# Optimization experiments

Measured on AMD Instinct MI355X. Metric: run time of the kernel, lower is better.

## Reference

```python
import jax, jax.numpy as jnp
import numpy as np

# G graphs of K atoms each, fully connected within graph (no self loops)
G, K, L, H, F, EMB, HID = 256, 16, 3, 3, 64, 200, 256
N = G * K
E = G * K * (K - 1)


def _wap(x, index, weights, num_seg, pw, gW1, gb1, gW2, gb2, mW1, mb1, mW2, mb2):
    """Roost WeightedAttentionPooling: segment softmax of gate_nn(x), scaled by
    weights**pow, applied to message_nn(x), segment-summed."""
    gate = jax.nn.selu(x @ gW1 + gb1) @ gW2 + gb2                      # [M]
    gmax = jax.ops.segment_max(gate, index, num_segments=num_seg)      # [S]
    gate = jnp.power(weights, pw) * jnp.exp(gate - gmax[index])        # [M]
    den = jax.ops.segment_sum(gate, index, num_segments=num_seg) + 1e-10
    attn = gate / den[index]                                           # [M]
    msg = jax.nn.selu(x @ mW1 + mb1) @ mW2 + mb2                       # [M,F]
    return jax.ops.segment_sum(attn[:, None] * msg, index, num_segments=num_seg)


def _wap_heads(x, index, weights, num_seg, params):
    f = lambda pw, gW1, gb1, gW2, gb2, mW1, mb1, mW2, mb2: _wap(
        x, index, weights, num_seg, pw, gW1, gb1, gW2, gb2, mW1, mb1, mW2, mb2)
    return jax.vmap(f)(*params)                                        # [H,S,F]


def setup_inputs() -> dict:
    key = jax.random.key(0)
    ks = jax.random.split(key, 16)
    # graph structure
    batch = jnp.repeat(jnp.arange(G, dtype=jnp.int32), K)              # [N]
    i = np.arange(K)
    src, dst = np.meshgrid(i, i, indexing="ij")
    mask = src != dst
    src, dst = src[mask], dst[mask]                                    # [K*(K-1)]
    offs = (np.arange(G) * K)[:, None]
    self_idx = jnp.asarray((offs + src[None, :]).reshape(-1), jnp.int32)
    nbr_idx = jnp.asarray((offs + dst[None, :]).reshape(-1), jnp.int32)

    s = lambda k, shape, fan_in: jax.random.normal(k, shape, jnp.float32) * (1.0 / fan_in) ** 0.5
    return dict(
        elem_weights=jax.random.uniform(ks[0], (N,), jnp.float32, 0.01, 1.0),
        elem_fea_in=jax.random.normal(ks[1], (N, EMB), jnp.float32),
        W_init=s(ks[2], (EMB, F - 1), EMB),
        b_init=jnp.zeros((F - 1,), jnp.float32),
        mg_W1=s(ks[3], (L, H, 2 * F, HID), 2 * F),
        mg_b1=jnp.zeros((L, H, HID), jnp.float32),
        mg_W2=s(ks[4], (L, H, HID), HID),
        mg_b2=jnp.zeros((L, H), jnp.float32),
        mm_W1=s(ks[5], (L, H, 2 * F, HID), 2 * F),
        mm_b1=jnp.zeros((L, H, HID), jnp.float32),
        mm_W2=s(ks[6], (L, H, HID, F), HID),
        mm_b2=jnp.zeros((L, H, F), jnp.float32),
        m_pow=jax.random.normal(ks[7], (L, H), jnp.float32),
        cg_W1=s(ks[8], (H, F, HID), F),
        cg_b1=jnp.zeros((H, HID), jnp.float32),
        cg_W2=s(ks[9], (H, HID), HID),
        cg_b2=jnp.zeros((H,), jnp.float32),
        cm_W1=s(ks[10], (H, F, HID), F),
        cm_b1=jnp.zeros((H, HID), jnp.float32),
        cm_W2=s(ks[11], (H, HID, F), HID),
        cm_b2=jnp.zeros((H, F), jnp.float32),
        c_pow=jax.random.normal(ks[12], (H,), jnp.float32),
        batch=batch,
        self_idx=self_idx,
        nbr_idx=nbr_idx,
    )


def reference(elem_weights, elem_fea_in, W_init, b_init,
              mg_W1, mg_b1, mg_W2, mg_b2, mm_W1, mm_b1, mm_W2, mm_b2, m_pow,
              cg_W1, cg_b1, cg_W2, cg_b2, cm_W1, cm_b1, cm_W2, cm_b2, c_pow,
              batch, self_idx, nbr_idx):
    w = elem_weights                                                   # [N]
    # initial embed: Linear(EMB, F-1) then concat fractional weight
    fea = jnp.concatenate([elem_fea_in @ W_init + b_init, w[:, None]], -1)  # [N,F]
    wn = w[nbr_idx]                                                    # [E]
    for l in range(L):
        pair = jnp.concatenate([fea[self_idx], fea[nbr_idx]], -1)      # [E,2F]
        heads = _wap_heads(pair, self_idx, wn, N,
                           (m_pow[l], mg_W1[l], mg_b1[l], mg_W2[l], mg_b2[l],
                            mm_W1[l], mm_b1[l], mm_W2[l], mm_b2[l]))   # [H,N,F]
        fea = fea + heads.mean(0)                                      # residual
    cry = _wap_heads(fea, batch, w, G,
                     (c_pow, cg_W1, cg_b1, cg_W2, cg_b2,
                      cm_W1, cm_b1, cm_W2, cm_b2))                     # [H,G,F]
    return cry.mean(0)                                                 # [G,F]
```

## Files before the change

kernel.cpp:

```cpp
#include <hip/hip_runtime.h>
#include <hip/hip_bf16.h>

#define G_ 256
#define K_ 16
#define L_ 3
#define H_ 3
#define F_ 64
#define EMB_ 200
#define HID_ 256
#define N_ (G_*K_)

typedef __attribute__((ext_vector_type(8))) short short8;
typedef __attribute__((ext_vector_type(4))) float f32x4;

#define SELU_S 1.0507009873554804934193349852946f
#define SELU_SA (1.0507009873554804934193349852946f*1.6732632423543772848170429916717f)
#define LOG2E_ 1.4426950408889634073599246810019f
#define SLN2_ (SELU_S*0.69314718055994530941723212145818f)

__device__ __forceinline__ float exp2_fast(float x) {
#if __has_builtin(__builtin_amdgcn_exp2f)
  return __builtin_amdgcn_exp2f(x);
#else
  return __exp2f(x);
#endif
}

__device__ __forceinline__ float selu_t(float t) {
  float tn = fminf(t, 0.f), tp = fmaxf(t, 0.f);
  return fmaf(SELU_SA, exp2_fast(tn), fmaf(SLN2_, tp, -SELU_SA));
}

__device__ __forceinline__ float selu_f(float x) {
  float e = __expf(x);
  float neg = fmaf(SELU_SA, e, -SELU_SA);
  float pos = SELU_S * x;
  return x > 0.f ? pos : neg;
}

__device__ __forceinline__ unsigned short f2bf(float x) {
  __hip_bfloat16 h = __float2bfloat16(x);
  return *reinterpret_cast<unsigned short*>(&h);
}

__device__ __forceinline__ unsigned int f2bf2(float a, float b) {
  float2 t; t.x = a; t.y = b;
  __hip_bfloat162 h = __float22bfloat162_rn(t);
  return *reinterpret_cast<unsigned int*>(&h);
}

__device__ __forceinline__ float bf2f(unsigned short u) {
  union { unsigned int i; float f; } v;
  v.i = ((unsigned int)u) << 16;
  return v.f;
}

__global__ __launch_bounds__(256) void prep_init_all(
    const float* __restrict__ mg_W1, const float* __restrict__ mm_W1,
    const float* __restrict__ mm_W2, const float* __restrict__ cg_W1,
    const float* __restrict__ cm_W1, const float* __restrict__ cm_W2,
    const float* __restrict__ mg_b1, const float* __restrict__ mm_b1,
    const float* __restrict__ cg_b1, const float* __restrict__ cm_b1,
    unsigned short* __restrict__ WcatT, unsigned short* __restrict__ W2mT,
    unsigned short* __restrict__ WcryT, unsigned short* __restrict__ W2cT,
    float* __restrict__ bias_e, float* __restrict__ bias_c,
    float* __restrict__ out0, float* __restrict__ feaZ,
    const float* __restrict__ fea_in, const float* __restrict__ W_init,
    const float* __restrict__ b_init, const float* __restrict__ wts,
    float* __restrict__ feaA) {
  int bid = blockIdx.x, tid = threadIdx.x;
  if (bid >= 256) {
    __shared__ float row[4][EMB_];
    int sub = tid >> 6, j = tid & 63;
    int n = (bid - 256) * 4 + sub;
    for (int k = j; k < EMB_; k += 64) row[sub][k] = fea_in[(size_t)n*EMB_ + k];
    __syncthreads();
    if (j < F_-1) {
      float s = b_init[j];
      for (int k = 0; k < EMB_; ++k) s = fmaf(row[sub][k], W_init[k*(F_-1) + j], s);
      feaA[(size_t)n*F_ + j] = s;
    } else {
      feaA[(size_t)n*F_ + (F_-1)] = wts[n];
    }
    return;
  }
  int gt = bid*256 + tid, GT = 256*256;
  for (int idx = gt; idx < 9*1024*64; idx += GT) {
    int lh = idx >> 16, n = (idx >> 6) & 1023, k = idx & 63;
    const float* W = (n < 512) ? mg_W1 : mm_W1;
    int nn = n & 511;
    int r = (nn < 256) ? k : (64 + k);
    WcatT[idx] = f2bf(W[(size_t)lh*(2*F_*HID_) + r*HID_ + (nn & 255)]);
  }
  for (int idx = gt; idx < 9*64*256; idx += GT) {
    int lh = idx >> 14, f = (idx >> 8) & 63, k = idx & 255;
    W2mT[idx] = f2bf(mm_W2[(size_t)lh*(HID_*F_) + k*F_ + f]);
  }
  for (int idx = gt; idx < 1536*64; idx += GT) {
    int n = idx >> 6, k = idx & 63;
    int hh = n >> 9, r = n & 511;
    float v = (r < 256) ? cg_W1[(size_t)hh*F_*HID_ + k*HID_ + r]
                        : cm_W1[(size_t)hh*F_*HID_ + k*HID_ + (r - 256)];
    WcryT[idx] = f2bf(v);
  }
  for (int idx = gt; idx < 3*64*256; idx += GT) {
    int hh = idx >> 14, f = (idx >> 8) & 63, k = idx & 255;
    W2cT[idx] = f2bf(cm_W2[(size_t)hh*HID_*F_ + k*F_ + f]);
  }
  for (int idx = gt; idx < 9216 + 1536 + G_*F_; idx += GT) {
    if (idx < 9216) {
      int l = idx / 3072, c = idx - l*3072;
      int hh = c >> 10, cc = c & 1023;
      int lh = l*H_ + hh;
      float v = 0.f;
      if (cc < 256) v = mg_b1[lh*HID_ + cc];
      else if (cc >= 512 && cc < 768) v = mm_b1[lh*HID_ + (cc - 512)];
      bias_e[idx] = v;
    } else if (idx < 9216 + 1536) {
      int c = idx - 9216;
      int hh = c >> 9, cc = c & 511;
      bias_c[c] = (cc < 256) ? cg_b1[hh*HID_ + cc] : cm_b1[hh*HID_ + (cc - 256)];
    } else {
      out0[idx - 9216 - 1536] = 0.f;
    }
  }
  float4 z4; z4.x = 0.f; z4.y = 0.f; z4.z = 0.f; z4.w = 0.f;
  for (int idx = gt; idx < (3*N_*F_)/4; idx += GT)
    ((float4*)feaZ)[idx] = z4;
}

__global__ __launch_bounds__(512, 4) void edge_fused(
    const float* __restrict__ fea, const unsigned short* __restrict__ WcatT,
    const float* __restrict__ bias_e, const unsigned short* __restrict__ W2T,
    const float* __restrict__ mg_W2, const float* __restrict__ mg_b2,
    const float* __restrict__ m_pow, const float* __restrict__ mm_b2,
    const float* __restrict__ wts, float* __restrict__ fea_nxt, int l) {
  __shared__ __align__(16) unsigned short feaS[16][72];
  __shared__ __align__(16) unsigned short PQs[16][520];
  __shared__ __align__(16) unsigned short HbarS[16][264];
  __shared__ float bs[512];
  __shared__ float w2g[256];
  __shared__ float gred[240][2];
  __shared__ float gateA[240];
  __shared__ float sumat[16];
  __shared__ float wp[16];
  int t = threadIdx.x;
  int g = blockIdx.x, g16 = g * 16;
  int h = blockIdx.y, lh = l*H_ + h;
  const unsigned short* Wlh = WcatT + (size_t)lh*1024*64;
  const float* biaslh = bias_e + (size_t)l*3072 + h*1024;
  int w = t >> 6, lane = t & 63, mr = lane & 15, q = lane >> 4;

  {
    int row = t >> 5, c2 = (t & 31) * 2;
    float2 fv = *(const float2*)&fea[(size_t)(g16 + row)*64 + c2];
    *(unsigned int*)&feaS[row][c2] = f2bf2(fv.x, fv.y);
  }
  bs[t] = biaslh[t];
  if (t < 256) w2g[t] = mg_W2[lh*HID_ + t];
  __syncthreads();

  {
    int n0w = w * 64;
    short8 a0 = *(const short8*)&feaS[mr][q*8];
    short8 a1 = *(const short8*)&feaS[mr][32 + q*8];
    #pragma unroll
    for (int nt = 0; nt < 4; ++nt) {
      int n = n0w + nt*16 + mr;
      const unsigned short* bp = Wlh + (size_t)n*64 + q*8;
      short8 b0 = *(const short8*)bp;
      short8 b1 = *(const short8*)(bp + 32);
      f32x4 z = {0.f, 0.f, 0.f, 0.f};
      z = __builtin_amdgcn_mfma_f32_16x16x32_bf16(a0, b0, z, 0, 0, 0);
      z = __builtin_amdgcn_mfma_f32_16x16x32_bf16(a1, b1, z, 0, 0, 0);
      float bb = bs[n];
      #pragma unroll
      for (int r = 0; r < 4; ++r)
        PQs[q*4 + r][n] = f2bf(z[r] + bb);
    }
  }
  __syncthreads();

  {
    float nb = biaslh[512 + t];
    if (t < 480) {
      int e = t >> 1, half = t & 1;
      int i = e / 15, jj = e - i*15;
      int j = (jj < i) ? jj : jj + 1;
      float s = 0.f;
      #pragma unroll
      for (int u = 0; u < 16; ++u) {
        int c = half*8 + u*16;
        short8 pv = *(const short8*)&PQs[i][c];
        short8 qv = *(const short8*)&PQs[j][256 + c];
        #pragma unroll
        for (int r = 0; r < 8; ++r) {
          float hv = selu_f(bf2f((unsigned short)pv[r]) + bf2f((unsigned short)qv[r]));
          s = fmaf(hv, w2g[c + r], s);
        }
      }
      gred[e][half] = s;
    } else if (t < 496) {
      wp[t - 480] = __powf(wts[g16 + (t - 480)], m_pow[lh]);
    }
    bs[t] = nb;
  }
  __syncthreads();

  {
    int n0w = w * 64;
    short8 a0 = *(const short8*)&feaS[mr][q*8];
    short8 a1 = *(const short8*)&feaS[mr][32 + q*8];
    #pragma unroll
    for (int nt = 0; nt < 4; ++nt) {
      int n = n0w + nt*16 + mr;
      const unsigned short* bp = Wlh + (size_t)(512 + n)*64 + q*8;
      short8 b0 = *(const short8*)bp;
      short8 b1 = *(const short8*)(bp + 32);
      f32x4 z = {0.f, 0.f, 0.f, 0.f};
      z = __builtin_amdgcn_mfma_f32_16x16x32_bf16(a0, b0, z, 0, 0, 0);
      z = __builtin_amdgcn_mfma_f32_16x16x32_bf16(a1, b1, z, 0, 0, 0);
      float bb = bs[n];
      #pragma unroll
      for (int r = 0; r < 4; ++r)
        PQs[q*4 + r][n] = f2bf(z[r] + bb);
    }
  }
  if (t < 16) {
    int i = t;
    float b2v = mg_b2[lh];
    float gl[15];
    float m = -1e30f;
    #pragma unroll
    for (int jj = 0; jj < 15; ++jj) {
      float v = gred[i*15 + jj][0] + gred[i*15 + jj][1] + b2v;
      gl[jj] = v; m = fmaxf(m, v);
    }
    float den = 0.f;
    #pragma unroll
    for (int jj = 0; jj < 15; ++jj) {
      int j = (jj < i) ? jj : jj + 1;
      float x = wp[j] * __expf(gl[jj] - m);
      gl[jj] = x; den += x;
    }
    den += 1e-10f;
    float sa = 0.f;
    #pragma unroll
    for (int jj = 0; jj < 15; ++jj) {
      float a = gl[jj] / den; gateA[i*15 + jj] = a; sa += a;
    }
    sumat[i] = sa;
  }
  __syncthreads();

  {
    int i = t >> 5, k0 = (t & 31) * 8;
    short8 pv = *(const short8*)&PQs[i][k0];
    float pf[8];
    #pragma unroll
    for (int r = 0; r < 8; ++r) pf[r] = bf2f((unsigned short)pv[r]);
    float hb[8] = {0.f, 0.f, 0.f, 0.f, 0.f, 0.f, 0.f, 0.f};
    for (int jj = 0; jj < 15; ++jj) {
      int j = (jj < i) ? jj : jj + 1;
      float a = gateA[i*15 + jj];
      short8 qv = *(const short8*)&PQs[j][256 + k0];
      #pragma unroll
      for (int r = 0; r < 8; ++r) {
        float hv = selu_f(pf[r] + bf2f((unsigned short)qv[r]));
        hb[r] = fmaf(a, hv, hb[r]);
      }
    }
    unsigned int hpk[4];
    #pragma unroll
    for (int r2 = 0; r2 < 4; ++r2) hpk[r2] = f2bf2(hb[2*r2], hb[2*r2+1]);
    *(short8*)&HbarS[i][k0] = *reinterpret_cast<short8*>(hpk);
  }
  __syncthreads();

  if (w < 4) {
    const unsigned short* W2lh = W2T + (size_t)lh*64*256;
    f32x4 acc = {0.f, 0.f, 0.f, 0.f};
    #pragma unroll
    for (int kc = 0; kc < 8; ++kc) {
      short8 a = *(const short8*)&HbarS[mr][kc*32 + q*8];
      short8 b = *(const short8*)&W2lh[(size_t)(w*16 + mr)*256 + kc*32 + q*8];
      acc = __builtin_amdgcn_mfma_f32_16x16x32_bf16(a, b, acc, 0, 0, 0);
    }
    int f = w*16 + mr;
    float b2 = mm_b2[lh*F_ + f];
    #pragma unroll
    for (int r = 0; r < 4; ++r) {
      int i = q*4 + r;
      float val = (acc[r] + b2*sumat[i]) * (1.f/3.f);
      if (h == 0) val += fea[(size_t)(g16 + i)*64 + f];
      atomicAdd(&fea_nxt[(size_t)(g16 + i)*64 + f], val);
    }
  }
}

__global__ __launch_bounds__(256) void cry_fused(
    const float* __restrict__ fea, const unsigned short* __restrict__ WcryT,
    const float* __restrict__ bias_c, const unsigned short* __restrict__ W2cT,
    const float* __restrict__ cg_W2, const float* __restrict__ cg_b2,
    const float* __restrict__ cm_b2, const float* __restrict__ c_pow,
    const float* __restrict__ wts, float* __restrict__ out) {
  __shared__ __align__(16) unsigned short feaS[16][72];
  __shared__ float PQh[16][520];
  __shared__ float bsc[512];
  __shared__ float gred[16][18];
  __shared__ float attnL[16];
  __shared__ float sumatS;
  __shared__ __align__(16) unsigned short hidc[16][264];
  int t = threadIdx.x;
  int g = blockIdx.x, g16 = g*16, h = blockIdx.y;
  {
    int row = t >> 4, c4 = (t & 15) * 4;
    float4 fv = *(const float4*)&fea[(size_t)(g16 + row)*64 + c4];
    *(unsigned int*)&feaS[row][c4]   = f2bf2(fv.x, fv.y);
    *(unsigned int*)&feaS[row][c4+2] = f2bf2(fv.z, fv.w);
  }
  bsc[t] = bias_c[h*512 + t];
  bsc[256 + t] = bias_c[h*512 + 256 + t];
  int w = t >> 6, lane = t & 63, mr = lane & 15, q = lane >> 4;
  __syncthreads();
  {
    int n0w = w * 128;
    short8 a0 = *(const short8*)&feaS[mr][q*8];
    short8 a1 = *(const short8*)&feaS[mr][32 + q*8];
    #pragma unroll
    for (int nt = 0; nt < 8; ++nt) {
      int n = n0w + nt*16 + mr;
      const unsigned short* bp = WcryT + (size_t)(h*512 + n)*64 + q*8;
      short8 b0 = *(const short8*)bp;
      short8 b1 = *(const short8*)(bp + 32);
      f32x4 z = {0.f, 0.f, 0.f, 0.f};
      z = __builtin_amdgcn_mfma_f32_16x16x32_bf16(a0, b0, z, 0, 0, 0);
      z = __builtin_amdgcn_mfma_f32_16x16x32_bf16(a1, b1, z, 0, 0, 0);
      float bb = bsc[n];
      #pragma unroll
      for (int r = 0; r < 4; ++r)
        PQh[q*4 + r][n] = (z[r] + bb) * LOG2E_;
    }
  }
  __syncthreads();
  {
    int i = t >> 4, c0 = (t & 15) * 16;
    float s = 0.f;
    #pragma unroll
    for (int c = c0; c < c0+16; ++c)
      s = fmaf(selu_t(PQh[i][c]), cg_W2[h*HID_ + c], s);
    gred[i][t & 15] = s;
  }
  __syncthreads();
  if (t < 16) {
    float sg = 0.f;
    #pragma unroll
    for (int u2 = 0; u2 < 16; ++u2) sg += gred[t][u2];
    gred[t][16] = sg + cg_b2[h];
  }
  __syncthreads();
  if (t == 0) {
    float pw = c_pow[h];
    float m = -1e30f;
    #pragma unroll
    for (int i = 0; i < 16; ++i) m = fmaxf(m, gred[i][16]);
    float den = 0.f; float v[16];
    #pragma unroll
    for (int i = 0; i < 16; ++i) {
      float x = __powf(wts[g16+i], pw) * __expf(gred[i][16] - m);
      v[i] = x; den += x;
    }
    den += 1e-10f;
    float sa = 0.f;
    #pragma unroll
    for (int i = 0; i < 16; ++i) { float a = v[i]/den; attnL[i] = a; sa += a; }
    sumatS = sa;
  }
  {
    int i = t >> 4, c0 = (t & 15) * 16;
    #pragma unroll
    for (int c = c0; c < c0+16; c += 2) {
      unsigned int pk = f2bf2(selu_t(PQh[i][256 + c]), selu_t(PQh[i][256 + c + 1]));
      *(unsigned int*)&hidc[i][c] = pk;
    }
  }
  __syncthreads();
  f32x4 acc = {0.f, 0.f, 0.f, 0.f};
  #pragma unroll
  for (int kc = 0; kc < 8; ++kc) {
    short8 a = *(const short8*)&hidc[mr][kc*32 + q*8];
    short8 b = *(const short8*)&W2cT[((size_t)h*64 + w*16 + mr)*HID_ + kc*32 + q*8];
    acc = __builtin_amdgcn_mfma_f32_16x16x32_bf16(a, b, acc, 0, 0, 0);
  }
  float p = 0.f;
  #pragma unroll
  for (int r = 0; r < 4; ++r) p = fmaf(attnL[q*4+r], acc[r], p);
  p += __shfl_xor(p, 16);
  p += __shfl_xor(p, 32);
  if (q == 0) {
    int f = w*16 + mr;
    atomicAdd(&out[(size_t)g*64 + f],
              (p + cm_b2[h*F_ + f]*sumatS) * (1.f/(float)H_));
  }
}

extern "C" void kernel_launch(void* const* d_in, const int* in_sizes, int n_in,
                              void* d_out, int out_size, void* d_ws, size_t ws_size,
                              hipStream_t stream) {
  const float* elem_weights = (const float*)d_in[0];
  const float* elem_fea_in  = (const float*)d_in[1];
  const float* W_init = (const float*)d_in[2];
  const float* b_init = (const float*)d_in[3];
  const float* mg_W1  = (const float*)d_in[4];
  const float* mg_b1  = (const float*)d_in[5];
  const float* mg_W2  = (const float*)d_in[6];
  const float* mg_b2  = (const float*)d_in[7];
  const float* mm_W1  = (const float*)d_in[8];
  const float* mm_b1  = (const float*)d_in[9];
  const float* mm_W2  = (const float*)d_in[10];
  const float* mm_b2  = (const float*)d_in[11];
  const float* m_pow  = (const float*)d_in[12];
  const float* cg_W1  = (const float*)d_in[13];
  const float* cg_b1  = (const float*)d_in[14];
  const float* cg_W2  = (const float*)d_in[15];
  const float* cg_b2  = (const float*)d_in[16];
  const float* cm_W1  = (const float*)d_in[17];
  const float* cm_b1  = (const float*)d_in[18];
  const float* cm_W2  = (const float*)d_in[19];
  const float* cm_b2  = (const float*)d_in[20];
  const float* c_pow  = (const float*)d_in[21];
  float* out = (float*)d_out;

  float* ws = (float*)d_ws;
  float* feaA  = ws;
  float* feaB  = feaA + (size_t)N_*F_;
  float* feaC  = feaB + (size_t)N_*F_;
  float* feaD  = feaC + (size_t)N_*F_;
  unsigned short* WcatT = (unsigned short*)(feaD + (size_t)N_*F_);
  unsigned short* W2mT  = WcatT + (size_t)9*1024*64;
  unsigned short* WcryT = W2mT  + (size_t)9*64*256;
  unsigned short* W2cT  = WcryT + (size_t)1536*64;
  float* bias_e = (float*)(W2cT + (size_t)3*64*256);
  float* bias_c = bias_e + 9216;

  prep_init_all<<<256 + N_/4, 256, 0, stream>>>(
      mg_W1, mm_W1, mm_W2, cg_W1, cm_W1, cm_W2,
      mg_b1, mm_b1, cg_b1, cm_b1,
      WcatT, W2mT, WcryT, W2cT, bias_e, bias_c,
      out, feaB,
      elem_fea_in, W_init, b_init, elem_weights, feaA);

  float* bufs[4] = {feaA, feaB, feaC, feaD};
  for (int l = 0; l < L_; ++l) {
    edge_fused<<<dim3(G_, H_), 512, 0, stream>>>(
        bufs[l], WcatT, bias_e, W2mT, mg_W2, mg_b2, m_pow, mm_b2,
        elem_weights, bufs[l+1], l);
  }

  cry_fused<<<dim3(G_, H_), 256, 0, stream>>>(
      bufs[3], WcryT, bias_c, W2cT, cg_W2, cg_b2, cm_b2, c_pow,
      elem_weights, out);
}
```

Measured before the change: 235.7 us.

## Fuse edge layers and crystal pooling into one kernel with per-graph barriers

The three edge_fused launches and the cry_fused launch are merged into a single net_fused kernel. The three head blocks of each graph synchronise through a global atomic counter with spin-waiting, which removes kernel-launch gaps and tail effects between layers. The crystal stage is reworked to run with 512 threads, store its hidden activations in bf16 and compute the softmax with shuffles instead of a single thread. The prep kernel now spreads its weight-transpose loops across all blocks and zeroes the counters. The spin barrier relies on all blocks of a graph being resident at the same time, so it risks deadlock if occupancy is insufficient.

```diff
diff --git a/kernel.cpp b/kernel.cpp
--- a/kernel.cpp
+++ b/kernel.cpp
@@ -53,6 +53,18 @@
   union { unsigned int i; float f; } v;
   v.i = ((unsigned int)u) << 16;
   return v.f;
+}
+
+__device__ __forceinline__ void graph_barrier(unsigned int* c, int t) {
+  __syncthreads();
+  if (t == 0) {
+    __threadfence();
+    atomicAdd(c, 1u);
+    while (__hip_atomic_load(c, __ATOMIC_ACQUIRE, __HIP_MEMORY_SCOPE_AGENT) < 3u)
+      __builtin_amdgcn_s_sleep(8);
+  }
+  __syncthreads();
+  __threadfence();
 }
 
 __global__ __launch_bounds__(256) void prep_init_all(
@@ -67,7 +79,7 @@
     float* __restrict__ out0, float* __restrict__ feaZ,
     const float* __restrict__ fea_in, const float* __restrict__ W_init,
     const float* __restrict__ b_init, const float* __restrict__ wts,
-    float* __restrict__ feaA) {
+    float* __restrict__ feaA, unsigned int* __restrict__ cnt0) {
   int bid = blockIdx.x, tid = threadIdx.x;
   if (bid >= 256) {
     __shared__ float row[4][EMB_];
@@ -82,9 +94,8 @@
     } else {
       feaA[(size_t)n*F_ + (F_-1)] = wts[n];
     }
-    return;
-  }
-  int gt = bid*256 + tid, GT = 256*256;
+  }
+  int gt = bid*256 + tid, GT = gridDim.x*256;
   for (int idx = gt; idx < 9*1024*64; idx += GT) {
     int lh = idx >> 16, n = (idx >> 6) & 1023, k = idx & 63;
     const float* W = (n < 512) ? mg_W1 : mm_W1;
@@ -107,7 +118,7 @@
     int hh = idx >> 14, f = (idx >> 8) & 63, k = idx & 255;
     W2cT[idx] = f2bf(cm_W2[(size_t)hh*HID_*F_ + k*F_ + f]);
   }
-  for (int idx = gt; idx < 9216 + 1536 + G_*F_; idx += GT) {
+  for (int idx = gt; idx < 9216 + 1536 + G_*F_ + 1024; idx += GT) {
     if (idx < 9216) {
       int l = idx / 3072, c = idx - l*3072;
       int hh = c >> 10, cc = c & 1023;
@@ -120,8 +131,10 @@
       int c = idx - 9216;
       int hh = c >> 9, cc = c & 511;
       bias_c[c] = (cc < 256) ? cg_b1[hh*HID_ + cc] : cm_b1[hh*HID_ + (cc - 256)];
+    } else if (idx < 9216 + 1536 + G_*F_) {
+      out0[idx - 9216 - 1536] = 0.f;
     } else {
-      out0[idx - 9216 - 1536] = 0.f;
+      cnt0[idx - 9216 - 1536 - G_*F_] = 0u;
     }
   }
   float4 z4; z4.x = 0.f; z4.y = 0.f; z4.z = 0.f; z4.w = 0.f;
@@ -129,41 +142,54 @@
     ((float4*)feaZ)[idx] = z4;
 }
 
-__global__ __launch_bounds__(512, 4) void edge_fused(
-    const float* __restrict__ fea, const unsigned short* __restrict__ WcatT,
-    const float* __restrict__ bias_e, const unsigned short* __restrict__ W2T,
-    const float* __restrict__ mg_W2, const float* __restrict__ mg_b2,
-    const float* __restrict__ m_pow, const float* __restrict__ mm_b2,
-    const float* __restrict__ wts, float* __restrict__ fea_nxt, int l) {
-  __shared__ __align__(16) unsigned short feaS[16][72];
-  __shared__ __align__(16) unsigned short PQs[16][520];
-  __shared__ __align__(16) unsigned short HbarS[16][264];
-  __shared__ float bs[512];
-  __shared__ float w2g[256];
-  __shared__ float gred[240][2];
-  __shared__ float gateA[240];
-  __shared__ float sumat[16];
-  __shared__ float wp[16];
-  int t = threadIdx.x;
-  int g = blockIdx.x, g16 = g * 16;
-  int h = blockIdx.y, lh = l*H_ + h;
+struct EdgeSmem {
+  unsigned short feaS[16][72];
+  unsigned short PQs[16][520];
+  unsigned short HbarS[16][264];
+  float bs[512];
+  float w2g[256];
+  float gred[240][2];
+  float gateA[240];
+  float sumat[16];
+  float wp[16];
+};
+struct CrySmem {
+  unsigned short feaS[16][72];
+  unsigned short PQh[16][520];
+  unsigned short hidc[16][264];
+  float bsc[512];
+  float gred[16][36];
+  float attnL[16];
+  float sumatS;
+};
+union NetSmem { EdgeSmem e; CrySmem c; };
+
+__device__ __forceinline__ void do_layer(
+    NetSmem& S, int t, int g16, int h, int l,
+    const float* __restrict__ cur, float* __restrict__ nxt,
+    const unsigned short* __restrict__ WcatT, const float* __restrict__ bias_e,
+    const unsigned short* __restrict__ W2T, const float* __restrict__ mg_W2,
+    const float* __restrict__ mg_b2, const float* __restrict__ m_pow,
+    const float* __restrict__ mm_b2, const float* __restrict__ wts) {
+  EdgeSmem& e = S.e;
+  int lh = l*H_ + h;
   const unsigned short* Wlh = WcatT + (size_t)lh*1024*64;
   const float* biaslh = bias_e + (size_t)l*3072 + h*1024;
   int w = t >> 6, lane = t & 63, mr = lane & 15, q = lane >> 4;
 
   {
     int row = t >> 5, c2 = (t & 31) * 2;
-    float2 fv = *(const float2*)&fea[(size_t)(g16 + row)*64 + c2];
-    *(unsigned int*)&feaS[row][c2] = f2bf2(fv.x, fv.y);
-  }
-  bs[t] = biaslh[t];
-  if (t < 256) w2g[t] = mg_W2[lh*HID_ + t];
+    float2 fv = *(const float2*)&cur[(size_t)(g16 + row)*64 + c2];
+    *(unsigned int*)&e.feaS[row][c2] = f2bf2(fv.x, fv.y);
+  }
+  e.bs[t] = biaslh[t];
+  if (t < 256) e.w2g[t] = mg_W2[lh*HID_ + t];
   __syncthreads();
 
   {
     int n0w = w * 64;
-    short8 a0 = *(const short8*)&feaS[mr][q*8];
-    short8 a1 = *(const short8*)&feaS[mr][32 + q*8];
+    short8 a0 = *(const short8*)&e.feaS[mr][q*8];
+    short8 a1 = *(const short8*)&e.feaS[mr][32 + q*8];
     #pragma unroll
     for (int nt = 0; nt < 4; ++nt) {
       int n = n0w + nt*16 + mr;
@@ -173,10 +199,10 @@
       f32x4 z = {0.f, 0.f, 0.f, 0.f};
       z = __builtin_amdgcn_mfma_f32_16x16x32_bf16(a0, b0, z, 0, 0, 0);
       z = __builtin_amdgcn_mfma_f32_16x16x32_bf16(a1, b1, z, 0, 0, 0);
-      float bb = bs[n];
+      float bb = e.bs[n];
       #pragma unroll
       for (int r = 0; r < 4; ++r)
-        PQs[q*4 + r][n] = f2bf(z[r] + bb);
+        e.PQs[q*4 + r][n] = f2bf(z[r] + bb);
     }
   }
   __syncthreads();
@@ -184,33 +210,33 @@
   {
     float nb = biaslh[512 + t];
     if (t < 480) {
-      int e = t >> 1, half = t & 1;
-      int i = e / 15, jj = e - i*15;
+      int ed = t >> 1, half = t & 1;
+      int i = ed / 15, jj = ed - i*15;
       int j = (jj < i) ? jj : jj + 1;
       float s = 0.f;
       #pragma unroll
       for (int u = 0; u < 16; ++u) {
         int c = half*8 + u*16;
-        short8 pv = *(const short8*)&PQs[i][c];
-        short8 qv = *(const short8*)&PQs[j][256 + c];
+        short8 pv = *(const short8*)&e.PQs[i][c];
+        short8 qv = *(const short8*)&e.PQs[j][256 + c];
         #pragma unroll
         for (int r = 0; r < 8; ++r) {
           float hv = selu_f(bf2f((unsigned short)pv[r]) + bf2f((unsigned short)qv[r]));
-          s = fmaf(hv, w2g[c + r], s);
+          s = fmaf(hv, e.w2g[c + r], s);
         }
       }
-      gred[e][half] = s;
+      e.gred[ed][half] = s;
     } else if (t < 496) {
-      wp[t - 480] = __powf(wts[g16 + (t - 480)], m_pow[lh]);
-    }
-    bs[t] = nb;
+      e.wp[t - 480] = __powf(wts[g16 + (t - 480)], m_pow[lh]);
+    }
+    e.bs[t] = nb;
   }
   __syncthreads();
 
   {
     int n0w = w * 64;
-    short8 a0 = *(const short8*)&feaS[mr][q*8];
-    short8 a1 = *(const short8*)&feaS[mr][32 + q*8];
+    short8 a0 = *(const short8*)&e.feaS[mr][q*8];
+    short8 a1 = *(const short8*)&e.feaS[mr][32 + q*8];
     #pragma unroll
     for (int nt = 0; nt < 4; ++nt) {
       int n = n0w + nt*16 + mr;
@@ -220,10 +246,10 @@
       f32x4 z = {0.f, 0.f, 0.f, 0.f};
       z = __builtin_amdgcn_mfma_f32_16x16x32_bf16(a0, b0, z, 0, 0, 0);
       z = __builtin_amdgcn_mfma_f32_16x16x32_bf16(a1, b1, z, 0, 0, 0);
-      float bb = bs[n];
+      float bb = e.bs[n];
       #pragma unroll
       for (int r = 0; r < 4; ++r)
-        PQs[q*4 + r][n] = f2bf(z[r] + bb);
+        e.PQs[q*4 + r][n] = f2bf(z[r] + bb);
     }
   }
   if (t < 16) {
@@ -233,37 +259,37 @@
     float m = -1e30f;
     #pragma unroll
     for (int jj = 0; jj < 15; ++jj) {
-      float v = gred[i*15 + jj][0] + gred[i*15 + jj][1] + b2v;
+      float v = e.gred[i*15 + jj][0] + e.gred[i*15 + jj][1] + b2v;
       gl[jj] = v; m = fmaxf(m, v);
     }
     float den = 0.f;
     #pragma unroll
     for (int jj = 0; jj < 15; ++jj) {
       int j = (jj < i) ? jj : jj + 1;
-      float x = wp[j] * __expf(gl[jj] - m);
+      float x = e.wp[j] * __expf(gl[jj] - m);
       gl[jj] = x; den += x;
     }
     den += 1e-10f;
     float sa = 0.f;
     #pragma unroll
     for (int jj = 0; jj < 15; ++jj) {
-      float a = gl[jj] / den; gateA[i*15 + jj] = a; sa += a;
-    }
-    sumat[i] = sa;
+      float a = gl[jj] / den; e.gateA[i*15 + jj] = a; sa += a;
+    }
+    e.sumat[i] = sa;
   }
   __syncthreads();
 
   {
     int i = t >> 5, k0 = (t & 31) * 8;
-    short8 pv = *(const short8*)&PQs[i][k0];
+    short8 pv = *(const short8*)&e.PQs[i][k0];
     float pf[8];
     #pragma unroll
     for (int r = 0; r < 8; ++r) pf[r] = bf2f((unsigned short)pv[r]);
     float hb[8] = {0.f, 0.f, 0.f, 0.f, 0.f, 0.f, 0.f, 0.f};
     for (int jj = 0; jj < 15; ++jj) {
       int j = (jj < i) ? jj : jj + 1;
-      float a = gateA[i*15 + jj];
-      short8 qv = *(const short8*)&PQs[j][256 + k0];
+      float a = e.gateA[i*15 + jj];
+      short8 qv = *(const short8*)&e.PQs[j][256 + k0];
       #pragma unroll
       for (int r = 0; r < 8; ++r) {
         float hv = selu_f(pf[r] + bf2f((unsigned short)qv[r]));
@@ -273,7 +299,7 @@
     unsigned int hpk[4];
     #pragma unroll
     for (int r2 = 0; r2 < 4; ++r2) hpk[r2] = f2bf2(hb[2*r2], hb[2*r2+1]);
-    *(short8*)&HbarS[i][k0] = *reinterpret_cast<short8*>(hpk);
+    *(short8*)&e.HbarS[i][k0] = *reinterpret_cast<short8*>(hpk);
   }
   __syncthreads();
 
@@ -282,7 +308,7 @@
     f32x4 acc = {0.f, 0.f, 0.f, 0.f};
     #pragma unroll
     for (int kc = 0; kc < 8; ++kc) {
-      short8 a = *(const short8*)&HbarS[mr][kc*32 + q*8];
+      short8 a = *(const short8*)&e.HbarS[mr][kc*32 + q*8];
       short8 b = *(const short8*)&W2lh[(size_t)(w*16 + mr)*256 + kc*32 + q*8];
       acc = __builtin_amdgcn_mfma_f32_16x16x32_bf16(a, b, acc, 0, 0, 0);
     }
@@ -291,44 +317,36 @@
     #pragma unroll
     for (int r = 0; r < 4; ++r) {
       int i = q*4 + r;
-      float val = (acc[r] + b2*sumat[i]) * (1.f/3.f);
-      if (h == 0) val += fea[(size_t)(g16 + i)*64 + f];
-      atomicAdd(&fea_nxt[(size_t)(g16 + i)*64 + f], val);
-    }
-  }
-}
-
-__global__ __launch_bounds__(256) void cry_fused(
+      float val = (acc[r] + b2*e.sumat[i]) * (1.f/3.f);
+      if (h == 0) val += cur[(size_t)(g16 + i)*64 + f];
+      atomicAdd(&nxt[(size_t)(g16 + i)*64 + f], val);
+    }
+  }
+}
+
+__device__ __forceinline__ void do_cry(
+    NetSmem& S, int t, int g, int h,
     const float* __restrict__ fea, const unsigned short* __restrict__ WcryT,
     const float* __restrict__ bias_c, const unsigned short* __restrict__ W2cT,
     const float* __restrict__ cg_W2, const float* __restrict__ cg_b2,
     const float* __restrict__ cm_b2, const float* __restrict__ c_pow,
     const float* __restrict__ wts, float* __restrict__ out) {
-  __shared__ __align__(16) unsigned short feaS[16][72];
-  __shared__ float PQh[16][520];
-  __shared__ float bsc[512];
-  __shared__ float gred[16][18];
-  __shared__ float attnL[16];
-  __shared__ float sumatS;
-  __shared__ __align__(16) unsigned short hidc[16][264];
-  int t = threadIdx.x;
-  int g = blockIdx.x, g16 = g*16, h = blockIdx.y;
-  {
-    int row = t >> 4, c4 = (t & 15) * 4;
-    float4 fv = *(const float4*)&fea[(size_t)(g16 + row)*64 + c4];
-    *(unsigned int*)&feaS[row][c4]   = f2bf2(fv.x, fv.y);
-    *(unsigned int*)&feaS[row][c4+2] = f2bf2(fv.z, fv.w);
-  }
-  bsc[t] = bias_c[h*512 + t];
-  bsc[256 + t] = bias_c[h*512 + 256 + t];
+  CrySmem& c = S.c;
+  int g16 = g*16;
   int w = t >> 6, lane = t & 63, mr = lane & 15, q = lane >> 4;
-  __syncthreads();
-  {
-    int n0w = w * 128;
-    short8 a0 = *(const short8*)&feaS[mr][q*8];
-    short8 a1 = *(const short8*)&feaS[mr][32 + q*8];
-    #pragma unroll
-    for (int nt = 0; nt < 8; ++nt) {
+  {
+    int row = t >> 5, c2 = (t & 31) * 2;
+    float2 fv = *(const float2*)&fea[(size_t)(g16 + row)*64 + c2];
+    *(unsigned int*)&c.feaS[row][c2] = f2bf2(fv.x, fv.y);
+  }
+  c.bsc[t] = bias_c[h*512 + t];
+  __syncthreads();
+  {
+    int n0w = w * 64;
+    short8 a0 = *(const short8*)&c.feaS[mr][q*8];
+    short8 a1 = *(const short8*)&c.feaS[mr][32 + q*8];
+    #pragma unroll
+    for (int nt = 0; nt < 4; ++nt) {
       int n = n0w + nt*16 + mr;
       const unsigned short* bp = WcryT + (size_t)(h*512 + n)*64 + q*8;
       short8 b0 = *(const short8*)bp;
@@ -336,72 +354,98 @@
       f32x4 z = {0.f, 0.f, 0.f, 0.f};
       z = __builtin_amdgcn_mfma_f32_16x16x32_bf16(a0, b0, z, 0, 0, 0);
       z = __builtin_amdgcn_mfma_f32_16x16x32_bf16(a1, b1, z, 0, 0, 0);
-      float bb = bsc[n];
+      float bb = c.bsc[n];
       #pragma unroll
       for (int r = 0; r < 4; ++r)
-        PQh[q*4 + r][n] = (z[r] + bb) * LOG2E_;
-    }
-  }
-  __syncthreads();
-  {
-    int i = t >> 4, c0 = (t & 15) * 16;
+        c.PQh[q*4 + r][n] = f2bf((z[r] + bb) * LOG2E_);
+    }
+  }
+  __syncthreads();
+  {
+    int i = t >> 5, c0 = (t & 31) * 8;
     float s = 0.f;
     #pragma unroll
-    for (int c = c0; c < c0+16; ++c)
-      s = fmaf(selu_t(PQh[i][c]), cg_W2[h*HID_ + c], s);
-    gred[i][t & 15] = s;
+    for (int cc = c0; cc < c0+8; ++cc)
+      s = fmaf(selu_t(bf2f(c.PQh[i][cc])), cg_W2[h*HID_ + cc], s);
+    c.gred[i][t & 31] = s;
   }
   __syncthreads();
   if (t < 16) {
     float sg = 0.f;
     #pragma unroll
-    for (int u2 = 0; u2 < 16; ++u2) sg += gred[t][u2];
-    gred[t][16] = sg + cg_b2[h];
-  }
-  __syncthreads();
-  if (t == 0) {
-    float pw = c_pow[h];
-    float m = -1e30f;
-    #pragma unroll
-    for (int i = 0; i < 16; ++i) m = fmaxf(m, gred[i][16]);
-    float den = 0.f; float v[16];
-    #pragma unroll
-    for (int i = 0; i < 16; ++i) {
-      float x = __powf(wts[g16+i], pw) * __expf(gred[i][16] - m);
-      v[i] = x; den += x;
-    }
-    den += 1e-10f;
-    float sa = 0.f;
-    #pragma unroll
-    for (int i = 0; i < 16; ++i) { float a = v[i]/den; attnL[i] = a; sa += a; }
-    sumatS = sa;
-  }
-  {
-    int i = t >> 4, c0 = (t & 15) * 16;
-    #pragma unroll
-    for (int c = c0; c < c0+16; c += 2) {
-      unsigned int pk = f2bf2(selu_t(PQh[i][256 + c]), selu_t(PQh[i][256 + c + 1]));
-      *(unsigned int*)&hidc[i][c] = pk;
-    }
-  }
-  __syncthreads();
-  f32x4 acc = {0.f, 0.f, 0.f, 0.f};
-  #pragma unroll
-  for (int kc = 0; kc < 8; ++kc) {
-    short8 a = *(const short8*)&hidc[mr][kc*32 + q*8];
-    short8 b = *(const short8*)&W2cT[((size_t)h*64 + w*16 + mr)*HID_ + kc*32 + q*8];
-    acc = __builtin_amdgcn_mfma_f32_16x16x32_bf16(a, b, acc, 0, 0, 0);
-  }
-  float p = 0.f;
-  #pragma unroll
-  for (int r = 0; r < 4; ++r) p = fmaf(attnL[q*4+r], acc[r], p);
-  p += __shfl_xor(p, 16);
-  p += __shfl_xor(p, 32);
-  if (q == 0) {
-    int f = w*16 + mr;
-    atomicAdd(&out[(size_t)g*64 + f],
-              (p + cm_b2[h*F_ + f]*sumatS) * (1.f/(float)H_));
-  }
+    for (int u = 0; u < 32; ++u) sg += c.gred[t][u];
+    sg += cg_b2[h];
+    float m = sg;
+    #pragma unroll
+    for (int s = 1; s < 16; s <<= 1) m = fmaxf(m, __shfl_xor(m, s, 16));
+    float x = __powf(wts[g16 + t], c_pow[h]) * __expf(sg - m);
+    float d = x;
+    #pragma unroll
+    for (int s = 1; s < 16; s <<= 1) d += __shfl_xor(d, s, 16);
+    d += 1e-10f;
+    float a = x / d;
+    c.attnL[t] = a;
+    float sa = a;
+    #pragma unroll
+    for (int s = 1; s < 16; s <<= 1) sa += __shfl_xor(sa, s, 16);
+    if (t == 0) c.sumatS = sa;
+  }
+  {
+    int i = t >> 5, c0 = (t & 31) * 8;
+    #pragma unroll
+    for (int cc = c0; cc < c0+8; cc += 2) {
+      unsigned int pk = f2bf2(selu_t(bf2f(c.PQh[i][256 + cc])),
+                              selu_t(bf2f(c.PQh[i][256 + cc + 1])));
+      *(unsigned int*)&c.hidc[i][cc] = pk;
+    }
+  }
+  __syncthreads();
+  if (w < 4) {
+    f32x4 acc = {0.f, 0.f, 0.f, 0.f};
+    #pragma unroll
+    for (int kc = 0; kc < 8; ++kc) {
+      short8 a = *(const short8*)&c.hidc[mr][kc*32 + q*8];
+      short8 b = *(const short8*)&W2cT[((size_t)h*64 + w*16 + mr)*HID_ + kc*32 + q*8];
+      acc = __builtin_amdgcn_mfma_f32_16x16x32_bf16(a, b, acc, 0, 0, 0);
+    }
+    float p = 0.f;
+    #pragma unroll
+    for (int r = 0; r < 4; ++r) p = fmaf(c.attnL[q*4+r], acc[r], p);
+    p += __shfl_xor(p, 16);
+    p += __shfl_xor(p, 32);
+    if (q == 0) {
+      int f = w*16 + mr;
+      atomicAdd(&out[(size_t)g*64 + f],
+                (p + cm_b2[h*F_ + f]*c.sumatS) * (1.f/(float)H_));
+    }
+  }
+}
+
+__global__ __launch_bounds__(512, 8) void net_fused(
+    const float* __restrict__ fea0, float* __restrict__ fea1,
+    float* __restrict__ fea2, float* __restrict__ fea3,
+    const unsigned short* __restrict__ WcatT, const float* __restrict__ bias_e,
+    const unsigned short* __restrict__ W2mT, const float* __restrict__ mg_W2,
+    const float* __restrict__ mg_b2, const float* __restrict__ m_pow,
+    const float* __restrict__ mm_b2,
+    const unsigned short* __restrict__ WcryT, const float* __restrict__ bias_c,
+    const unsigned short* __restrict__ W2cT, const float* __restrict__ cg_W2,
+    const float* __restrict__ cg_b2, const float* __restrict__ cm_b2,
+    const float* __restrict__ c_pow,
+    const float* __restrict__ wts, float* __restrict__ out,
+    unsigned int* __restrict__ cnt) {
+  __shared__ __align__(16) NetSmem sm;
+  int t = threadIdx.x;
+  int g = blockIdx.x, g16 = g*16;
+  int h = blockIdx.y;
+
+  do_layer(sm, t, g16, h, 0, fea0, fea1, WcatT, bias_e, W2mT, mg_W2, mg_b2, m_pow, mm_b2, wts);
+  graph_barrier(&cnt[g*4 + 0], t);
+  do_layer(sm, t, g16, h, 1, fea1, fea2, WcatT, bias_e, W2mT, mg_W2, mg_b2, m_pow, mm_b2, wts);
+  graph_barrier(&cnt[g*4 + 1], t);
+  do_layer(sm, t, g16, h, 2, fea2, fea3, WcatT, bias_e, W2mT, mg_W2, mg_b2, m_pow, mm_b2, wts);
+  graph_barrier(&cnt[g*4 + 2], t);
+  do_cry(sm, t, g, h, fea3, WcryT, bias_c, W2cT, cg_W2, cg_b2, cm_b2, c_pow, wts, out);
 }
 
 extern "C" void kernel_launch(void* const* d_in, const int* in_sizes, int n_in,
@@ -442,22 +486,18 @@
   unsigned short* W2cT  = WcryT + (size_t)1536*64;
   float* bias_e = (float*)(W2cT + (size_t)3*64*256);
   float* bias_c = bias_e + 9216;
+  unsigned int* cnt = (unsigned int*)(bias_c + 1536);
 
   prep_init_all<<<256 + N_/4, 256, 0, stream>>>(
       mg_W1, mm_W1, mm_W2, cg_W1, cm_W1, cm_W2,
       mg_b1, mm_b1, cg_b1, cm_b1,
       WcatT, W2mT, WcryT, W2cT, bias_e, bias_c,
       out, feaB,
-      elem_fea_in, W_init, b_init, elem_weights, feaA);
-
-  float* bufs[4] = {feaA, feaB, feaC, feaD};
-  for (int l = 0; l < L_; ++l) {
-    edge_fused<<<dim3(G_, H_), 512, 0, stream>>>(
-        bufs[l], WcatT, bias_e, W2mT, mg_W2, mg_b2, m_pow, mm_b2,
-        elem_weights, bufs[l+1], l);
-  }
-
-  cry_fused<<<dim3(G_, H_), 256, 0, stream>>>(
-      bufs[3], WcryT, bias_c, W2cT, cg_W2, cg_b2, cm_b2, c_pow,
-      elem_weights, out);
-}
+      elem_fea_in, W_init, b_init, elem_weights, feaA, cnt);
+
+  net_fused<<<dim3(G_, H_), 512, 0, stream>>>(
+      feaA, feaB, feaC, feaD,
+      WcatT, bias_e, W2mT, mg_W2, mg_b2, m_pow, mm_b2,
+      WcryT, bias_c, W2cT, cg_W2, cg_b2, cm_b2, c_pow,
+      elem_weights, out, cnt);
+}
```

Result: slower. 694.8 us (+194.8%).

## Split edge kernel across two blocks per graph by target-atom halves

Applied to the files above, without the earlier changes.

Each graph/head is now handled by two 256-thread blocks, each owning 8 of the 16 target atoms, instead of one 512-thread block. Both blocks still compute the full P/Q projections, which are needed for every neighbor, so that GEMM work is duplicated. The pairwise gate, aggregation and output GEMM are halved per block, and the bias shared buffer is dropped in favor of direct global loads. The aim is more, smaller blocks for better occupancy and load balance. The cost is redundant projection compute and a half-empty 16-row MFMA in the final stage.

```diff
diff --git a/kernel.cpp b/kernel.cpp
--- a/kernel.cpp
+++ b/kernel.cpp
@@ -129,7 +129,7 @@
     ((float4*)feaZ)[idx] = z4;
 }
 
-__global__ __launch_bounds__(512, 4) void edge_fused(
+__global__ __launch_bounds__(256, 4) void edge_fused(
     const float* __restrict__ fea, const unsigned short* __restrict__ WcatT,
     const float* __restrict__ bias_e, const unsigned short* __restrict__ W2T,
     const float* __restrict__ mg_W2, const float* __restrict__ mg_b2,
@@ -137,35 +137,35 @@
     const float* __restrict__ wts, float* __restrict__ fea_nxt, int l) {
   __shared__ __align__(16) unsigned short feaS[16][72];
   __shared__ __align__(16) unsigned short PQs[16][520];
-  __shared__ __align__(16) unsigned short HbarS[16][264];
-  __shared__ float bs[512];
+  __shared__ __align__(16) unsigned short HbarS[8][264];
   __shared__ float w2g[256];
-  __shared__ float gred[240][2];
-  __shared__ float gateA[240];
-  __shared__ float sumat[16];
+  __shared__ float gred[120][2];
+  __shared__ float gateA[120];
+  __shared__ float sumat[8];
   __shared__ float wp[16];
   int t = threadIdx.x;
   int g = blockIdx.x, g16 = g * 16;
   int h = blockIdx.y, lh = l*H_ + h;
+  int i0 = blockIdx.z * 8;
   const unsigned short* Wlh = WcatT + (size_t)lh*1024*64;
   const float* biaslh = bias_e + (size_t)l*3072 + h*1024;
   int w = t >> 6, lane = t & 63, mr = lane & 15, q = lane >> 4;
 
   {
-    int row = t >> 5, c2 = (t & 31) * 2;
-    float2 fv = *(const float2*)&fea[(size_t)(g16 + row)*64 + c2];
-    *(unsigned int*)&feaS[row][c2] = f2bf2(fv.x, fv.y);
-  }
-  bs[t] = biaslh[t];
-  if (t < 256) w2g[t] = mg_W2[lh*HID_ + t];
-  __syncthreads();
-
-  {
-    int n0w = w * 64;
+    int row = t >> 4, c4 = (t & 15) * 4;
+    float4 fv = *(const float4*)&fea[(size_t)(g16 + row)*64 + c4];
+    *(unsigned int*)&feaS[row][c4]   = f2bf2(fv.x, fv.y);
+    *(unsigned int*)&feaS[row][c4+2] = f2bf2(fv.z, fv.w);
+  }
+  w2g[t] = mg_W2[lh*HID_ + t];
+  __syncthreads();
+
+  {
+    int n0w = w * 128;
     short8 a0 = *(const short8*)&feaS[mr][q*8];
     short8 a1 = *(const short8*)&feaS[mr][32 + q*8];
     #pragma unroll
-    for (int nt = 0; nt < 4; ++nt) {
+    for (int nt = 0; nt < 8; ++nt) {
       int n = n0w + nt*16 + mr;
       const unsigned short* bp = Wlh + (size_t)n*64 + q*8;
       short8 b0 = *(const short8*)bp;
@@ -173,7 +173,7 @@
       f32x4 z = {0.f, 0.f, 0.f, 0.f};
       z = __builtin_amdgcn_mfma_f32_16x16x32_bf16(a0, b0, z, 0, 0, 0);
       z = __builtin_amdgcn_mfma_f32_16x16x32_bf16(a1, b1, z, 0, 0, 0);
-      float bb = bs[n];
+      float bb = biaslh[n];
       #pragma unroll
       for (int r = 0; r < 4; ++r)
         PQs[q*4 + r][n] = f2bf(z[r] + bb);
@@ -182,16 +182,16 @@
   __syncthreads();
 
   {
-    float nb = biaslh[512 + t];
-    if (t < 480) {
-      int e = t >> 1, half = t & 1;
-      int i = e / 15, jj = e - i*15;
-      int j = (jj < i) ? jj : jj + 1;
+    if (t < 240) {
+      int e = t >> 1, ch = t & 1;
+      int il = e / 15, jj = e - il*15;
+      int ig = i0 + il;
+      int j = (jj < ig) ? jj : jj + 1;
       float s = 0.f;
       #pragma unroll
       for (int u = 0; u < 16; ++u) {
-        int c = half*8 + u*16;
-        short8 pv = *(const short8*)&PQs[i][c];
+        int c = ch*8 + u*16;
+        short8 pv = *(const short8*)&PQs[ig][c];
         short8 qv = *(const short8*)&PQs[j][256 + c];
         #pragma unroll
         for (int r = 0; r < 8; ++r) {
@@ -199,20 +199,19 @@
           s = fmaf(hv, w2g[c + r], s);
         }
       }
-      gred[e][half] = s;
-    } else if (t < 496) {
-      wp[t - 480] = __powf(wts[g16 + (t - 480)], m_pow[lh]);
-    }
-    bs[t] = nb;
-  }
-  __syncthreads();
-
-  {
-    int n0w = w * 64;
+      gred[e][ch] = s;
+    } else {
+      wp[t - 240] = __powf(wts[g16 + (t - 240)], m_pow[lh]);
+    }
+  }
+  __syncthreads();
+
+  {
+    int n0w = w * 128;
     short8 a0 = *(const short8*)&feaS[mr][q*8];
     short8 a1 = *(const short8*)&feaS[mr][32 + q*8];
     #pragma unroll
-    for (int nt = 0; nt < 4; ++nt) {
+    for (int nt = 0; nt < 8; ++nt) {
       int n = n0w + nt*16 + mr;
       const unsigned short* bp = Wlh + (size_t)(512 + n)*64 + q*8;
       short8 b0 = *(const short8*)bp;
@@ -220,26 +219,26 @@
       f32x4 z = {0.f, 0.f, 0.f, 0.f};
       z = __builtin_amdgcn_mfma_f32_16x16x32_bf16(a0, b0, z, 0, 0, 0);
       z = __builtin_amdgcn_mfma_f32_16x16x32_bf16(a1, b1, z, 0, 0, 0);
-      float bb = bs[n];
+      float bb = biaslh[512 + n];
       #pragma unroll
       for (int r = 0; r < 4; ++r)
         PQs[q*4 + r][n] = f2bf(z[r] + bb);
     }
   }
-  if (t < 16) {
-    int i = t;
+  if (t < 8) {
+    int il = t, ig = i0 + il;
     float b2v = mg_b2[lh];
     float gl[15];
     float m = -1e30f;
     #pragma unroll
     for (int jj = 0; jj < 15; ++jj) {
-      float v = gred[i*15 + jj][0] + gred[i*15 + jj][1] + b2v;
+      float v = gred[il*15 + jj][0] + gred[il*15 + jj][1] + b2v;
       gl[jj] = v; m = fmaxf(m, v);
     }
     float den = 0.f;
     #pragma unroll
     for (int jj = 0; jj < 15; ++jj) {
-      int j = (jj < i) ? jj : jj + 1;
+      int j = (jj < ig) ? jj : jj + 1;
       float x = wp[j] * __expf(gl[jj] - m);
       gl[jj] = x; den += x;
     }
@@ -247,22 +246,22 @@
     float sa = 0.f;
     #pragma unroll
     for (int jj = 0; jj < 15; ++jj) {
-      float a = gl[jj] / den; gateA[i*15 + jj] = a; sa += a;
-    }
-    sumat[i] = sa;
-  }
-  __syncthreads();
-
-  {
-    int i = t >> 5, k0 = (t & 31) * 8;
-    short8 pv = *(const short8*)&PQs[i][k0];
+      float a = gl[jj] / den; gateA[il*15 + jj] = a; sa += a;
+    }
+    sumat[il] = sa;
+  }
+  __syncthreads();
+
+  {
+    int il = t >> 5, ig = i0 + il, k0 = (t & 31) * 8;
+    short8 pv = *(const short8*)&PQs[ig][k0];
     float pf[8];
     #pragma unroll
     for (int r = 0; r < 8; ++r) pf[r] = bf2f((unsigned short)pv[r]);
     float hb[8] = {0.f, 0.f, 0.f, 0.f, 0.f, 0.f, 0.f, 0.f};
     for (int jj = 0; jj < 15; ++jj) {
-      int j = (jj < i) ? jj : jj + 1;
-      float a = gateA[i*15 + jj];
+      int j = (jj < ig) ? jj : jj + 1;
+      float a = gateA[il*15 + jj];
       short8 qv = *(const short8*)&PQs[j][256 + k0];
       #pragma unroll
       for (int r = 0; r < 8; ++r) {
@@ -273,16 +272,16 @@
     unsigned int hpk[4];
     #pragma unroll
     for (int r2 = 0; r2 < 4; ++r2) hpk[r2] = f2bf2(hb[2*r2], hb[2*r2+1]);
-    *(short8*)&HbarS[i][k0] = *reinterpret_cast<short8*>(hpk);
-  }
-  __syncthreads();
-
-  if (w < 4) {
+    *(short8*)&HbarS[il][k0] = *reinterpret_cast<short8*>(hpk);
+  }
+  __syncthreads();
+
+  {
     const unsigned short* W2lh = W2T + (size_t)lh*64*256;
     f32x4 acc = {0.f, 0.f, 0.f, 0.f};
     #pragma unroll
     for (int kc = 0; kc < 8; ++kc) {
-      short8 a = *(const short8*)&HbarS[mr][kc*32 + q*8];
+      short8 a = *(const short8*)&HbarS[mr & 7][kc*32 + q*8];
       short8 b = *(const short8*)&W2lh[(size_t)(w*16 + mr)*256 + kc*32 + q*8];
       acc = __builtin_amdgcn_mfma_f32_16x16x32_bf16(a, b, acc, 0, 0, 0);
     }
@@ -290,10 +289,13 @@
     float b2 = mm_b2[lh*F_ + f];
     #pragma unroll
     for (int r = 0; r < 4; ++r) {
-      int i = q*4 + r;
-      float val = (acc[r] + b2*sumat[i]) * (1.f/3.f);
-      if (h == 0) val += fea[(size_t)(g16 + i)*64 + f];
-      atomicAdd(&fea_nxt[(size_t)(g16 + i)*64 + f], val);
+      int io = q*4 + r;
+      if (io < 8) {
+        int ig = i0 + io;
+        float val = (acc[r] + b2*sumat[io]) * (1.f/3.f);
+        if (h == 0) val += fea[(size_t)(g16 + ig)*64 + f];
+        atomicAdd(&fea_nxt[(size_t)(g16 + ig)*64 + f], val);
+      }
     }
   }
 }
@@ -452,7 +454,7 @@
 
   float* bufs[4] = {feaA, feaB, feaC, feaD};
   for (int l = 0; l < L_; ++l) {
-    edge_fused<<<dim3(G_, H_), 512, 0, stream>>>(
+    edge_fused<<<dim3(G_, H_, 2), 256, 0, stream>>>(
         bufs[l], WcatT, bias_e, W2mT, mg_W2, mg_b2, m_pow, mm_b2,
         elem_weights, bufs[l+1], l);
   }
```

Measured after the change: 259.7 us. +10.2%, slower.
